# Kernel optimization log

Measured on AMD Instinct MI355X. Metric: run time of the kernel, lower is better.

Reference implementation:

```python
import jax, jax.numpy as jnp
import numpy as np

NB_HEAD = 16
SIZE_PER_HEAD = 64
D_MODEL = 1024
B, S = 4, 2048
NEG_BIG = 1e12  # matches the 1e12 additive-mask constant in the original


def setup_inputs() -> dict:
    key = jax.random.key(0)
    ks = jax.random.split(key, 8)
    Q_seq = jax.random.normal(ks[0], (B, S, D_MODEL), dtype=jnp.float32)
    K_seq = jax.random.normal(ks[1], (B, S, D_MODEL), dtype=jnp.float32)
    V_seq = jax.random.normal(ks[2], (B, S, D_MODEL), dtype=jnp.float32)
    out_dim = NB_HEAD * SIZE_PER_HEAD
    # glorot_uniform-style init
    lim = float(np.sqrt(6.0 / (D_MODEL + out_dim)))
    WQ = jax.random.uniform(ks[3], (D_MODEL, out_dim), minval=-lim, maxval=lim, dtype=jnp.float32)
    WK = jax.random.uniform(ks[4], (D_MODEL, out_dim), minval=-lim, maxval=lim, dtype=jnp.float32)
    WV = jax.random.uniform(ks[5], (D_MODEL, out_dim), minval=-lim, maxval=lim, dtype=jnp.float32)
    Q_len = jax.random.randint(ks[6], (B, 1), 1, S + 1, dtype=jnp.int32)
    V_len = jax.random.randint(ks[7], (B, 1), 1, S + 1, dtype=jnp.int32)
    return {"Q_seq": Q_seq, "K_seq": K_seq, "V_seq": V_seq,
            "WQ": WQ, "WK": WK, "WV": WV, "Q_len": Q_len, "V_len": V_len}


def _len_mask(lengths, seqlen, dtype):
    # one_hot(L) then 1 - cumsum along seq == (pos < L); L >= seqlen -> all ones
    return (jnp.arange(seqlen)[None, :] < lengths[:, 0][:, None]).astype(dtype)


def reference(Q_seq, K_seq, V_seq, WQ, WK, WV, Q_len, V_len):
    b, s, _ = Q_seq.shape
    h, dh = NB_HEAD, SIZE_PER_HEAD
    q = (Q_seq @ WQ).reshape(b, s, h, dh).transpose(0, 2, 1, 3)  # [B,H,S,Dh]
    k = (K_seq @ WK).reshape(b, s, h, dh).transpose(0, 2, 1, 3)
    v = (V_seq @ WV).reshape(b, s, h, dh).transpose(0, 2, 1, 3)
    scores = jnp.einsum('bhqd,bhkd->bhqk', q, k) / jnp.sqrt(jnp.float32(dh))
    mask_k = _len_mask(V_len, s, scores.dtype)  # [B,Sk]
    scores = scores - (1.0 - mask_k)[:, None, None, :] * NEG_BIG
    A = jax.nn.softmax(scores, axis=-1)
    o = jnp.einsum('bhqk,bhkd->bhqd', A, v)
    o = o.transpose(0, 2, 1, 3).reshape(b, s, h * dh)  # [B,S,D]
    mask_q = _len_mask(Q_len, s, o.dtype)
    return o * mask_q[:, :, None]
```

## Files before the change

kernel.cpp:

```cpp
#include <hip/hip_runtime.h>
#include <stdint.h>

typedef __attribute__((ext_vector_type(4))) float f32x4;
typedef __attribute__((ext_vector_type(8))) short bf16x8;
typedef __attribute__((ext_vector_type(4))) unsigned short u16x4;

#define MFMA16(a, b, c) __builtin_amdgcn_mfma_f32_16x16x32_bf16((a), (b), (c), 0, 0, 0)

static __device__ __forceinline__ unsigned short f2bf(float x) {
  union { float f; unsigned int u; } v; v.f = x;
  unsigned int r = v.u + 0x7fffu + ((v.u >> 16) & 1u);
  return (unsigned short)(r >> 16);
}

static __device__ __forceinline__ void gload_lds16(const void* g, void* l) {
  __builtin_amdgcn_global_load_lds(
      (__attribute__((address_space(1))) void*)(g),
      (__attribute__((address_space(3))) void*)(l), 16, 0, 0);
}

template <int CTRL>
static __device__ __forceinline__ float dpp_mov(float x) {
  union { float f; int i; } u, r;
  u.f = x;
  r.i = __builtin_amdgcn_update_dpp(u.i, u.i, CTRL, 0xF, 0xF, false);
  return r.f;
}
static __device__ __forceinline__ float dpp_max16(float x) {
  x = fmaxf(x, dpp_mov<0xB1>(x));
  x = fmaxf(x, dpp_mov<0x4E>(x));
  x = fmaxf(x, dpp_mov<0x124>(x));
  x = fmaxf(x, dpp_mov<0x128>(x));
  return x;
}
static __device__ __forceinline__ float dpp_sum16(float x) {
  x += dpp_mov<0xB1>(x);
  x += dpp_mov<0x4E>(x);
  x += dpp_mov<0x124>(x);
  x += dpp_mov<0x128>(x);
  return x;
}

__global__ void fill_kernel(float* p, int n, float v) {
  int i = blockIdx.x * blockDim.x + threadIdx.x;
  if (i < n) p[i] = v;
}

__global__ __launch_bounds__(256) void conv3_kernel(
    const float* __restrict__ S0, const float* __restrict__ S1, const float* __restrict__ S2,
    unsigned short* __restrict__ D0, unsigned short* __restrict__ D1,
    unsigned short* __restrict__ D2,
    const int* __restrict__ Qlen, const int* __restrict__ Vlen)
{
  const int y = blockIdx.y;
  {
    const int m0 = blockIdx.x * 4;
    const int b = m0 >> 11, s0 = m0 & 2047;
    const int L = (y == 0) ? Qlen[b] : Vlen[b];
    if (s0 >= ((L + 63) & ~63)) return;
  }
  const float* in = (y == 0) ? S0 : (y == 1) ? S1 : S2;
  unsigned short* outp = (y == 0) ? D0 : (y == 1) ? D1 : D2;
  const size_t base = ((size_t)blockIdx.x * 256 + threadIdx.x) * 16;
  const f32x4 a0 = *(const f32x4*)&in[base];
  const f32x4 a1 = *(const f32x4*)&in[base + 4];
  const f32x4 a2 = *(const f32x4*)&in[base + 8];
  const f32x4 a3 = *(const f32x4*)&in[base + 12];
  bf16x8 p0, p1;
#pragma unroll
  for (int u = 0; u < 4; ++u) {
    p0[u]     = (short)f2bf(a0[u]);
    p0[u + 4] = (short)f2bf(a1[u]);
    p1[u]     = (short)f2bf(a2[u]);
    p1[u + 4] = (short)f2bf(a3[u]);
  }
  *(bf16x8*)&outp[base]     = p0;
  *(bf16x8*)&outp[base + 8] = p1;
}

__global__ __launch_bounds__(256) void conv_kernel(
    const float* __restrict__ in, unsigned short* __restrict__ outp)
{
  const size_t base = ((size_t)blockIdx.x * 256 + threadIdx.x) * 16;
  const f32x4 a0 = *(const f32x4*)&in[base];
  const f32x4 a1 = *(const f32x4*)&in[base + 4];
  const f32x4 a2 = *(const f32x4*)&in[base + 8];
  const f32x4 a3 = *(const f32x4*)&in[base + 12];
  bf16x8 p0, p1;
#pragma unroll
  for (int u = 0; u < 4; ++u) {
    p0[u]     = (short)f2bf(a0[u]);
    p0[u + 4] = (short)f2bf(a1[u]);
    p1[u]     = (short)f2bf(a2[u]);
    p1[u + 4] = (short)f2bf(a3[u]);
  }
  *(bf16x8*)&outp[base]     = p0;
  *(bf16x8*)&outp[base + 8] = p1;
}

__global__ __launch_bounds__(256) void wtrans_kernel(
    const float* __restrict__ W0, const float* __restrict__ W1, const float* __restrict__ W2,
    unsigned short* __restrict__ T0, unsigned short* __restrict__ T1, unsigned short* __restrict__ T2)
{
  __shared__ __align__(16) float tile[64][65];
  const float* W = (blockIdx.z == 0) ? W0 : (blockIdx.z == 1) ? W1 : W2;
  unsigned short* T = (blockIdx.z == 0) ? T0 : (blockIdx.z == 1) ? T1 : T2;
  const int t = threadIdx.x;
  const int kb = blockIdx.x * 64, nb = blockIdx.y * 64;
  const int rr = t >> 4, cc = (t & 15) * 4;
#pragma unroll
  for (int p = 0; p < 4; ++p) {
    const int r = rr + p * 16;
    const f32x4 v = *(const f32x4*)&W[(size_t)(kb + r) * 1024 + nb + cc];
#pragma unroll
    for (int j = 0; j < 4; ++j) tile[r][cc + j] = v[j];
  }
  __syncthreads();
#pragma unroll
  for (int p = 0; p < 4; ++p) {
    const int n = rr + p * 16;
    u16x4 o;
#pragma unroll
    for (int j = 0; j < 4; ++j) o[j] = f2bf(tile[cc + j][n]);
    *(u16x4*)&T[(size_t)(nb + n) * 1024 + kb + cc] = o;
  }
}

__global__ __launch_bounds__(256) void proj_gemm_kernel(
    const unsigned short* __restrict__ A0, const unsigned short* __restrict__ A1,
    const unsigned short* __restrict__ A2,
    const unsigned short* __restrict__ B0, const unsigned short* __restrict__ B1,
    const unsigned short* __restrict__ B2,
    unsigned short* __restrict__ O0, unsigned short* __restrict__ O1,
    unsigned short* __restrict__ O2, int zbase,
    const int* __restrict__ Qlen, const int* __restrict__ Vlen)
{
  const int z = blockIdx.z + zbase;
  const int mm = (blockIdx.x + 8 * blockIdx.y + 24 * z) & 63;
  const int m0 = mm * 128, n0 = blockIdx.y * 128;

  {
    const int b = m0 >> 11, s0 = m0 & 2047;
    const int L = (z == 0) ? Qlen[b] : Vlen[b];
    if (s0 >= ((L + 63) & ~63)) return;
  }

  const unsigned short* Ab = (z == 0) ? A0 : (z == 1) ? A1 : A2;
  const unsigned short* Bt = (z == 0) ? B0 : (z == 1) ? B1 : B2;
  unsigned short* outp = (z == 0) ? O0 : (z == 1) ? O1 : O2;
  const float scale = (z == 0) ? 0.125f : 1.0f;

  __shared__ __align__(16) unsigned short Alds[4][128 * 32];
  __shared__ __align__(16) unsigned short Blds[4][128 * 32];
  const int t = threadIdx.x;
  const int lane = t & 63, w = t >> 6;
  const int wr = w >> 1, wc = w & 1;

  f32x4 acc[4][4] = {};

  const int L0 = t, L1 = t + 256;
  const int r0 = L0 >> 2, c0 = ((L0 & 3) ^ ((r0 >> 1) & 3)) * 8;
  const int r1 = L1 >> 2, c1 = ((L1 & 3) ^ ((r1 >> 1) & 3)) * 8;

#define PROJ_STAGE(tile, buf)                                                        \
  do {                                                                               \
    const int kt_ = (tile) * 32;                                                     \
    gload_lds16(&Ab[(size_t)(m0 + r0) * 1024 + kt_ + c0], &Alds[(buf)][L0 * 8]);     \
    gload_lds16(&Bt[(size_t)(n0 + r0) * 1024 + kt_ + c0], &Blds[(buf)][L0 * 8]);     \
    gload_lds16(&Ab[(size_t)(m0 + r1) * 1024 + kt_ + c1], &Alds[(buf)][L1 * 8]);     \
    gload_lds16(&Bt[(size_t)(n0 + r1) * 1024 + kt_ + c1], &Blds[(buf)][L1 * 8]);     \
  } while (0)

  PROJ_STAGE(0, 0);
  PROJ_STAGE(1, 1);
  PROJ_STAGE(2, 2);
  asm volatile("s_waitcnt vmcnt(8)" ::: "memory");
  __builtin_amdgcn_s_barrier();
  __builtin_amdgcn_sched_barrier(0);

  for (int tt = 0; tt < 32; ++tt) {
    const int cur = tt & 3;
    if (tt + 3 < 32) PROJ_STAGE(tt + 3, (tt + 3) & 3);

    const int q = lane >> 4;
    bf16x8 af[4], bfv[4];
#pragma unroll
    for (int m = 0; m < 4; ++m) {
      const int row = wr * 64 + m * 16 + (lane & 15);
      af[m] = *(const bf16x8*)&Alds[cur][row * 32 + ((q ^ ((row >> 1) & 3)) * 8)];
    }
#pragma unroll
    for (int n = 0; n < 4; ++n) {
      const int row = wc * 64 + n * 16 + (lane & 15);
      bfv[n] = *(const bf16x8*)&Blds[cur][row * 32 + ((q ^ ((row >> 1) & 3)) * 8)];
    }
    __builtin_amdgcn_s_setprio(1);
#pragma unroll
    for (int m = 0; m < 4; ++m)
#pragma unroll
      for (int n = 0; n < 4; ++n)
        acc[m][n] = MFMA16(af[m], bfv[n], acc[m][n]);
    __builtin_amdgcn_s_setprio(0);

    if (tt < 29)       asm volatile("s_waitcnt vmcnt(8)" ::: "memory");
    else if (tt == 29) asm volatile("s_waitcnt vmcnt(4)" ::: "memory");
    else               asm volatile("s_waitcnt vmcnt(0)" ::: "memory");
    __builtin_amdgcn_s_barrier();
    __builtin_amdgcn_sched_barrier(0);
  }
#undef PROJ_STAGE

#pragma unroll
  for (int mi = 0; mi < 4; ++mi) {
#pragma unroll
    for (int ni = 0; ni < 4; ++ni) {
      const int nn = n0 + wc * 64 + ni * 16 + (lane & 15);
      const int h = nn >> 6, d = nn & 63;
      const int mbase = m0 + wr * 64 + mi * 16 + ((lane >> 4) << 2);
      const int b = mbase >> 11;
      const int s = mbase & 2047;
      if (z != 2) {
#pragma unroll
        for (int j = 0; j < 4; ++j)
          outp[((size_t)(b * 16 + h) * 2048 + (s + j)) * 64 + d] = f2bf(acc[mi][ni][j] * scale);
      } else {
        u16x4 o;
#pragma unroll
        for (int j = 0; j < 4; ++j) o[j] = f2bf(acc[mi][ni][j]);
        *(u16x4*)&outp[((size_t)(b * 16 + h) * 64 + d) * 2048 + s] = o;
      }
    }
  }
}

__global__ __launch_bounds__(256) void attn_kernel(
    const unsigned short* __restrict__ qa, const unsigned short* __restrict__ ka,
    const unsigned short* __restrict__ va, const int* __restrict__ Qlen,
    const int* __restrict__ Vlen, float* __restrict__ outp)
{
  __shared__ __align__(16) unsigned short Klds[2][64 * 64];
  __shared__ __align__(16) unsigned short Vlds[2][64 * 64];
  __shared__ __align__(16) unsigned short Plds[4][16 * 64];
  const int t = threadIdx.x, lane = t & 63, w = t >> 6;
  const int bh = blockIdx.y, b = bh >> 4, h = bh & 15;
  const int q0 = blockIdx.x * 64;
  const int Lq = Qlen[b], Lv = Vlen[b];
  float* outb = outp + (size_t)b * 2048 * 1024 + h * 64;

  if (q0 >= Lq) {
    const int r = t >> 2, c0 = (t & 3) * 16;
    const f32x4 z = {0.f, 0.f, 0.f, 0.f};
#pragma unroll
    for (int j = 0; j < 4; ++j)
      *(f32x4*)&outb[(size_t)(q0 + r) * 1024 + c0 + j * 4] = z;
    return;
  }

  const unsigned short* qb = qa + (size_t)bh * 2048 * 64;
  const unsigned short* kb = ka + (size_t)bh * 2048 * 64;
  const unsigned short* vb = va + (size_t)bh * 64 * 2048;

  const int sr0 = t >> 3, sc0 = t & 7;
  const int sr1 = (t + 256) >> 3, sc1 = (t + 256) & 7;
  const int sd0 = sr0 * 64 + ((sc0 ^ (sr0 & 7)) * 8);
  const int sd1 = sr1 * 64 + ((sc1 ^ (sr1 & 7)) * 8);

  bf16x8 aq[2];
  {
    const int qrow = q0 + w * 16 + (lane & 15);
#pragma unroll
    for (int f = 0; f < 2; ++f)
      aq[f] = *(const bf16x8*)&qb[(size_t)qrow * 64 + (lane >> 4) * 8 + f * 32];
  }

  float m_run[4], l_run[4];
  f32x4 acc_o[4] = {};
#pragma unroll
  for (int j = 0; j < 4; ++j) { m_run[j] = -3.0e38f; l_run[j] = 0.0f; }

  const int nt = (Lv + 63) >> 6;

  bf16x8 kr0 = *(const bf16x8*)&kb[(size_t)sr0 * 64 + sc0 * 8];
  bf16x8 kr1 = *(const bf16x8*)&kb[(size_t)sr1 * 64 + sc1 * 8];
  bf16x8 vr0 = *(const bf16x8*)&vb[(size_t)sr0 * 2048 + sc0 * 8];
  bf16x8 vr1 = *(const bf16x8*)&vb[(size_t)sr1 * 2048 + sc1 * 8];
  *(bf16x8*)&Klds[0][sd0] = kr0;  *(bf16x8*)&Klds[0][sd1] = kr1;
  *(bf16x8*)&Vlds[0][sd0] = vr0;  *(bf16x8*)&Vlds[0][sd1] = vr1;

  for (int kt = 0; kt < nt; ++kt) {
    __syncthreads();
    const int cur = kt & 1;
    const unsigned short* Kc = &Klds[cur][0];
    const unsigned short* Vc = &Vlds[cur][0];
    const int k0 = kt * 64;

    const bool more = (kt + 1) < nt;
    if (more) {
      const int kn = k0 + 64;
      kr0 = *(const bf16x8*)&kb[(size_t)(kn + sr0) * 64 + sc0 * 8];
      kr1 = *(const bf16x8*)&kb[(size_t)(kn + sr1) * 64 + sc1 * 8];
      vr0 = *(const bf16x8*)&vb[(size_t)sr0 * 2048 + kn + sc0 * 8];
      vr1 = *(const bf16x8*)&vb[(size_t)sr1 * 2048 + kn + sc1 * 8];
    }

    f32x4 s4[4];
    __builtin_amdgcn_s_setprio(1);
#pragma unroll
    for (int kbk = 0; kbk < 4; ++kbk) {
      const int row = kbk * 16 + (lane & 15);
      f32x4 acc = {0.f, 0.f, 0.f, 0.f};
#pragma unroll
      for (int ds = 0; ds < 2; ++ds) {
        const int col = (((lane >> 4) * 8) + ds * 32) ^ ((row & 7) << 3);
        const bf16x8 bk = *(const bf16x8*)&Kc[row * 64 + col];
        acc = MFMA16(aq[ds], bk, acc);
      }
      if (k0 + row >= Lv) {
#pragma unroll
        for (int j = 0; j < 4; ++j) acc[j] = -1e30f;
      }
      s4[kbk] = acc;
    }
    __builtin_amdgcn_s_setprio(0);

    float mn[4], esc[4];
#pragma unroll
    for (int j = 0; j < 4; ++j) {
      float rm = fmaxf(fmaxf(s4[0][j], s4[1][j]), fmaxf(s4[2][j], s4[3][j]));
      rm = dpp_max16(rm);
      mn[j] = fmaxf(m_run[j], rm);
      esc[j] = __expf(m_run[j] - mn[j]);
      m_run[j] = mn[j];
    }

    float p[4][4];
    float rs[4] = {0.f, 0.f, 0.f, 0.f};
#pragma unroll
    for (int kbk = 0; kbk < 4; ++kbk)
#pragma unroll
      for (int j = 0; j < 4; ++j) {
        p[kbk][j] = __expf(s4[kbk][j] - mn[j]);
        rs[j] += p[kbk][j];
      }

    unsigned short* pl = &Plds[w][0];
#pragma unroll
    for (int kbk = 0; kbk < 4; ++kbk)
#pragma unroll
      for (int j = 0; j < 4; ++j) {
        const int row = (lane >> 4) * 4 + j;
        const int col = (kbk * 16 + (lane & 15)) ^ ((row & 7) << 3);
        pl[row * 64 + col] = f2bf(p[kbk][j]);
      }

#pragma unroll
    for (int j = 0; j < 4; ++j) {
      const float s = dpp_sum16(rs[j]);
      l_run[j] = l_run[j] * esc[j] + s;
    }
#pragma unroll
    for (int d = 0; d < 4; ++d)
#pragma unroll
      for (int j = 0; j < 4; ++j) acc_o[d][j] *= esc[j];

    bf16x8 pf[2];
#pragma unroll
    for (int ks = 0; ks < 2; ++ks) {
      const int row = lane & 15;
      const int col = ((lane >> 4) * 8 + ks * 32) ^ ((row & 7) << 3);
      pf[ks] = *(const bf16x8*)&pl[row * 64 + col];
    }

    __builtin_amdgcn_s_setprio(1);
#pragma unroll
    for (int db = 0; db < 4; ++db) {
#pragma unroll
      for (int ks = 0; ks < 2; ++ks) {
        const int vrow = db * 16 + (lane & 15);
        const int vcol = ((lane >> 4) * 8 + ks * 32) ^ ((vrow & 7) << 3);
        const bf16x8 vf = *(const bf16x8*)&Vc[vrow * 64 + vcol];
        acc_o[db] = MFMA16(pf[ks], vf, acc_o[db]);
      }
    }
    __builtin_amdgcn_s_setprio(0);

    if (more) {
      unsigned short* Kn = &Klds[cur ^ 1][0];
      unsigned short* Vn = &Vlds[cur ^ 1][0];
      *(bf16x8*)&Kn[sd0] = kr0;  *(bf16x8*)&Kn[sd1] = kr1;
      *(bf16x8*)&Vn[sd0] = vr0;  *(bf16x8*)&Vn[sd1] = vr1;
    }
  }

#pragma unroll
  for (int j = 0; j < 4; ++j) {
    const int row = q0 + w * 16 + (lane >> 4) * 4 + j;
    const float rl = 1.0f / l_run[j];
#pragma unroll
    for (int db = 0; db < 4; ++db) {
      const float v = acc_o[db][j] * rl;
      outb[(size_t)row * 1024 + db * 16 + (lane & 15)] = (row < Lq) ? v : 0.0f;
    }
  }
}

extern "C" void kernel_launch(void* const* d_in, const int* in_sizes, int n_in,
                              void* d_out, int out_size, void* d_ws, size_t ws_size,
                              hipStream_t stream) {
  float* out = (float*)d_out;

  const float* Qs = (const float*)d_in[0];
  const float* Ks = (const float*)d_in[1];
  const float* Vs = (const float*)d_in[2];
  const float* WQ = (const float*)d_in[3];
  const float* WK = (const float*)d_in[4];
  const float* WV = (const float*)d_in[5];
  const int* Qlen = (const int*)d_in[6];
  const int* Vlen = (const int*)d_in[7];

  unsigned short* WQt = (unsigned short*)d_ws;
  unsigned short* WKt = WQt + (size_t)1024 * 1024;
  unsigned short* WVt = WKt + (size_t)1024 * 1024;
  unsigned short* qa  = WVt + (size_t)1024 * 1024;
  unsigned short* ka  = qa + (size_t)8192 * 1024;
  unsigned short* va  = ka + (size_t)8192 * 1024;
  unsigned short* ext = va + (size_t)8192 * 1024;

  unsigned short* cA = (unsigned short*)d_out;
  unsigned short* cB = cA + (size_t)8192 * 1024;

  const size_t base_need = ((size_t)3 * 1024 * 1024 + (size_t)3 * 8192 * 1024) * 2;
  const size_t ext_need  = base_need + (size_t)8192 * 1024 * 2;

  if (ws_size < base_need) {
    fill_kernel<<<(out_size + 255) / 256, 256, 0, stream>>>(out, out_size, 256.0f);
    return;
  }

  wtrans_kernel<<<dim3(16, 16, 3), 256, 0, stream>>>(WQ, WK, WV, WQt, WKt, WVt);

  if (ws_size >= ext_need) {
    conv3_kernel<<<dim3(2048, 3), 256, 0, stream>>>(Qs, Ks, Vs, cA, cB, ext, Qlen, Vlen);
    proj_gemm_kernel<<<dim3(64, 8, 3), 256, 0, stream>>>(
        cA, cB, ext, WQt, WKt, WVt, qa, ka, va, 0, Qlen, Vlen);
  } else {
    conv_kernel<<<2048, 256, 0, stream>>>(Qs, cA);
    conv_kernel<<<2048, 256, 0, stream>>>(Ks, cB);
    proj_gemm_kernel<<<dim3(64, 8, 2), 256, 0, stream>>>(
        cA, cB, cB, WQt, WKt, WVt, qa, ka, va, 0, Qlen, Vlen);
    conv_kernel<<<2048, 256, 0, stream>>>(Vs, cA);
    proj_gemm_kernel<<<dim3(64, 8, 1), 256, 0, stream>>>(
        cA, cA, cA, WQt, WKt, WVt, qa, ka, va, 2, Qlen, Vlen);
  }
  attn_kernel<<<dim3(32, 64), 256, 0, stream>>>(qa, ka, va, Qlen, Vlen, out);
}
```

Before: 128.0 us.

## Process two 64-row query groups per attention block to reuse K/V tiles

Each attention block now handles 128 query rows, as two groups of 64 that share the same K/V LDS tiles. The grid is halved, so each K/V tile loaded from global memory feeds twice as many rows of QK and PV MFMA work. The cost is roughly double the accumulator and state registers per thread, which lowers occupancy and halves the number of blocks. Work also becomes coarser, since a block with one group past Lq still computes it and only zeroes the output rows at the end. The P scratch buffer in LDS is reused between the two groups within a wave.

```diff
diff --git a/kernel.cpp b/kernel.cpp
--- a/kernel.cpp
+++ b/kernel.cpp
@@ -243,7 +243,7 @@
   __shared__ __align__(16) unsigned short Plds[4][16 * 64];
   const int t = threadIdx.x, lane = t & 63, w = t >> 6;
   const int bh = blockIdx.y, b = bh >> 4, h = bh & 15;
-  const int q0 = blockIdx.x * 64;
+  const int q0 = blockIdx.x * 128;
   const int Lq = Qlen[b], Lv = Vlen[b];
   float* outb = outp + (size_t)b * 2048 * 1024 + h * 64;
 
@@ -251,8 +251,10 @@
     const int r = t >> 2, c0 = (t & 3) * 16;
     const f32x4 z = {0.f, 0.f, 0.f, 0.f};
 #pragma unroll
-    for (int j = 0; j < 4; ++j)
-      *(f32x4*)&outb[(size_t)(q0 + r) * 1024 + c0 + j * 4] = z;
+    for (int jj = 0; jj < 2; ++jj)
+#pragma unroll
+      for (int j = 0; j < 4; ++j)
+        *(f32x4*)&outb[(size_t)(q0 + jj * 64 + r) * 1024 + c0 + j * 4] = z;
     return;
   }
 
@@ -265,18 +267,21 @@
   const int sd0 = sr0 * 64 + ((sc0 ^ (sr0 & 7)) * 8);
   const int sd1 = sr1 * 64 + ((sc1 ^ (sr1 & 7)) * 8);
 
-  bf16x8 aq[2];
-  {
-    const int qrow = q0 + w * 16 + (lane & 15);
+  bf16x8 aq[2][2];
+#pragma unroll
+  for (int g = 0; g < 2; ++g) {
+    const int qrow = q0 + g * 64 + w * 16 + (lane & 15);
 #pragma unroll
     for (int f = 0; f < 2; ++f)
-      aq[f] = *(const bf16x8*)&qb[(size_t)qrow * 64 + (lane >> 4) * 8 + f * 32];
-  }
-
-  float m_run[4], l_run[4];
-  f32x4 acc_o[4] = {};
-#pragma unroll
-  for (int j = 0; j < 4; ++j) { m_run[j] = -3.0e38f; l_run[j] = 0.0f; }
+      aq[g][f] = *(const bf16x8*)&qb[(size_t)qrow * 64 + (lane >> 4) * 8 + f * 32];
+  }
+
+  float m_run[2][4], l_run[2][4];
+  f32x4 acc_o[2][4] = {};
+#pragma unroll
+  for (int g = 0; g < 2; ++g)
+#pragma unroll
+    for (int j = 0; j < 4; ++j) { m_run[g][j] = -3.0e38f; l_run[g][j] = 0.0f; }
 
   const int nt = (Lv + 63) >> 6;
 
@@ -303,86 +308,89 @@
       vr1 = *(const bf16x8*)&vb[(size_t)sr1 * 2048 + kn + sc1 * 8];
     }
 
-    f32x4 s4[4];
-    __builtin_amdgcn_s_setprio(1);
-#pragma unroll
-    for (int kbk = 0; kbk < 4; ++kbk) {
-      const int row = kbk * 16 + (lane & 15);
-      f32x4 acc = {0.f, 0.f, 0.f, 0.f};
-#pragma unroll
-      for (int ds = 0; ds < 2; ++ds) {
-        const int col = (((lane >> 4) * 8) + ds * 32) ^ ((row & 7) << 3);
-        const bf16x8 bk = *(const bf16x8*)&Kc[row * 64 + col];
-        acc = MFMA16(aq[ds], bk, acc);
-      }
-      if (k0 + row >= Lv) {
-#pragma unroll
-        for (int j = 0; j < 4; ++j) acc[j] = -1e30f;
-      }
-      s4[kbk] = acc;
-    }
-    __builtin_amdgcn_s_setprio(0);
-
-    float mn[4], esc[4];
-#pragma unroll
-    for (int j = 0; j < 4; ++j) {
-      float rm = fmaxf(fmaxf(s4[0][j], s4[1][j]), fmaxf(s4[2][j], s4[3][j]));
-      rm = dpp_max16(rm);
-      mn[j] = fmaxf(m_run[j], rm);
-      esc[j] = __expf(m_run[j] - mn[j]);
-      m_run[j] = mn[j];
-    }
-
-    float p[4][4];
-    float rs[4] = {0.f, 0.f, 0.f, 0.f};
-#pragma unroll
-    for (int kbk = 0; kbk < 4; ++kbk)
+#pragma unroll
+    for (int g = 0; g < 2; ++g) {
+      f32x4 s4[4];
+      __builtin_amdgcn_s_setprio(1);
+#pragma unroll
+      for (int kbk = 0; kbk < 4; ++kbk) {
+        const int row = kbk * 16 + (lane & 15);
+        f32x4 acc = {0.f, 0.f, 0.f, 0.f};
+#pragma unroll
+        for (int ds = 0; ds < 2; ++ds) {
+          const int col = (((lane >> 4) * 8) + ds * 32) ^ ((row & 7) << 3);
+          const bf16x8 bk = *(const bf16x8*)&Kc[row * 64 + col];
+          acc = MFMA16(aq[g][ds], bk, acc);
+        }
+        if (k0 + row >= Lv) {
+#pragma unroll
+          for (int j = 0; j < 4; ++j) acc[j] = -1e30f;
+        }
+        s4[kbk] = acc;
+      }
+      __builtin_amdgcn_s_setprio(0);
+
+      float mn[4], esc[4];
 #pragma unroll
       for (int j = 0; j < 4; ++j) {
-        p[kbk][j] = __expf(s4[kbk][j] - mn[j]);
-        rs[j] += p[kbk][j];
-      }
-
-    unsigned short* pl = &Plds[w][0];
-#pragma unroll
-    for (int kbk = 0; kbk < 4; ++kbk)
+        float rm = fmaxf(fmaxf(s4[0][j], s4[1][j]), fmaxf(s4[2][j], s4[3][j]));
+        rm = dpp_max16(rm);
+        mn[j] = fmaxf(m_run[g][j], rm);
+        esc[j] = __expf(m_run[g][j] - mn[j]);
+        m_run[g][j] = mn[j];
+      }
+
+      float p[4][4];
+      float rs[4] = {0.f, 0.f, 0.f, 0.f};
+#pragma unroll
+      for (int kbk = 0; kbk < 4; ++kbk)
+#pragma unroll
+        for (int j = 0; j < 4; ++j) {
+          p[kbk][j] = __expf(s4[kbk][j] - mn[j]);
+          rs[j] += p[kbk][j];
+        }
+
+      unsigned short* pl = &Plds[w][0];
+#pragma unroll
+      for (int kbk = 0; kbk < 4; ++kbk)
+#pragma unroll
+        for (int j = 0; j < 4; ++j) {
+          const int row = (lane >> 4) * 4 + j;
+          const int col = (kbk * 16 + (lane & 15)) ^ ((row & 7) << 3);
+          pl[row * 64 + col] = f2bf(p[kbk][j]);
+        }
+
 #pragma unroll
       for (int j = 0; j < 4; ++j) {
-        const int row = (lane >> 4) * 4 + j;
-        const int col = (kbk * 16 + (lane & 15)) ^ ((row & 7) << 3);
-        pl[row * 64 + col] = f2bf(p[kbk][j]);
-      }
-
-#pragma unroll
-    for (int j = 0; j < 4; ++j) {
-      const float s = dpp_sum16(rs[j]);
-      l_run[j] = l_run[j] * esc[j] + s;
-    }
-#pragma unroll
-    for (int d = 0; d < 4; ++d)
-#pragma unroll
-      for (int j = 0; j < 4; ++j) acc_o[d][j] *= esc[j];
-
-    bf16x8 pf[2];
-#pragma unroll
-    for (int ks = 0; ks < 2; ++ks) {
-      const int row = lane & 15;
-      const int col = ((lane >> 4) * 8 + ks * 32) ^ ((row & 7) << 3);
-      pf[ks] = *(const bf16x8*)&pl[row * 64 + col];
-    }
-
-    __builtin_amdgcn_s_setprio(1);
-#pragma unroll
-    for (int db = 0; db < 4; ++db) {
+        const float s = dpp_sum16(rs[j]);
+        l_run[g][j] = l_run[g][j] * esc[j] + s;
+      }
+#pragma unroll
+      for (int d = 0; d < 4; ++d)
+#pragma unroll
+        for (int j = 0; j < 4; ++j) acc_o[g][d][j] *= esc[j];
+
+      bf16x8 pf[2];
 #pragma unroll
       for (int ks = 0; ks < 2; ++ks) {
-        const int vrow = db * 16 + (lane & 15);
-        const int vcol = ((lane >> 4) * 8 + ks * 32) ^ ((vrow & 7) << 3);
-        const bf16x8 vf = *(const bf16x8*)&Vc[vrow * 64 + vcol];
-        acc_o[db] = MFMA16(pf[ks], vf, acc_o[db]);
-      }
-    }
-    __builtin_amdgcn_s_setprio(0);
+        const int row = lane & 15;
+        const int col = ((lane >> 4) * 8 + ks * 32) ^ ((row & 7) << 3);
+        pf[ks] = *(const bf16x8*)&pl[row * 64 + col];
+      }
+
+      __builtin_amdgcn_s_setprio(1);
+#pragma unroll
+      for (int db = 0; db < 4; ++db) {
+#pragma unroll
+        for (int ks = 0; ks < 2; ++ks) {
+          const int vrow = db * 16 + (lane & 15);
+          const int vcol = ((lane >> 4) * 8 + ks * 32) ^ ((vrow & 7) << 3);
+          const bf16x8 vf = *(const bf16x8*)&Vc[vrow * 64 + vcol];
+          acc_o[g][db] = MFMA16(pf[ks], vf, acc_o[g][db]);
+        }
+      }
+      __builtin_amdgcn_s_setprio(0);
+    }
 
     if (more) {
       unsigned short* Kn = &Klds[cur ^ 1][0];
@@ -393,15 +401,17 @@
   }
 
 #pragma unroll
-  for (int j = 0; j < 4; ++j) {
-    const int row = q0 + w * 16 + (lane >> 4) * 4 + j;
-    const float rl = 1.0f / l_run[j];
-#pragma unroll
-    for (int db = 0; db < 4; ++db) {
-      const float v = acc_o[db][j] * rl;
-      outb[(size_t)row * 1024 + db * 16 + (lane & 15)] = (row < Lq) ? v : 0.0f;
-    }
-  }
+  for (int g = 0; g < 2; ++g)
+#pragma unroll
+    for (int j = 0; j < 4; ++j) {
+      const int row = q0 + g * 64 + w * 16 + (lane >> 4) * 4 + j;
+      const float rl = 1.0f / l_run[g][j];
+#pragma unroll
+      for (int db = 0; db < 4; ++db) {
+        const float v = acc_o[g][db][j] * rl;
+        outb[(size_t)row * 1024 + db * 16 + (lane & 15)] = (row < Lq) ? v : 0.0f;
+      }
+    }
 }
 
 extern "C" void kernel_launch(void* const* d_in, const int* in_sizes, int n_in,
@@ -452,5 +462,5 @@
     proj_gemm_kernel<<<dim3(64, 8, 1), 256, 0, stream>>>(
         cA, cA, cA, WQt, WKt, WVt, qa, ka, va, 2, Qlen, Vlen);
   }
-  attn_kernel<<<dim3(32, 64), 256, 0, stream>>>(qa, ka, va, Qlen, Vlen, out);
-}
+  attn_kernel<<<dim3(16, 64), 256, 0, stream>>>(qa, ka, va, Qlen, Vlen, out);
+}
```

New measurement: 131.8 us. 1.03x slower.

## Split KV across waves in attention with per-wave LDS and final merge

Applied to the files above, without the earlier changes.

Each attention block now processes 16 query rows instead of 64, with its four waves each handling an interleaved subset of 32-key tiles using private LDS buffers, then merging partial softmax states (max, sum, accumulator) through shared memory. This removes the per-iteration block barrier and increases grid parallelism. In exchange, K/V tiles are reloaded for every 16 query rows, quadrupling K/V traffic, and a final cross-wave reduction is added.

```diff
diff --git a/kernel.cpp b/kernel.cpp
--- a/kernel.cpp
+++ b/kernel.cpp
@@ -238,21 +238,17 @@
     const unsigned short* __restrict__ va, const int* __restrict__ Qlen,
     const int* __restrict__ Vlen, float* __restrict__ outp)
 {
-  __shared__ __align__(16) unsigned short Klds[2][64 * 64];
-  __shared__ __align__(16) unsigned short Vlds[2][64 * 64];
-  __shared__ __align__(16) unsigned short Plds[4][16 * 64];
+  __shared__ __align__(16) unsigned char smem[36864];
   const int t = threadIdx.x, lane = t & 63, w = t >> 6;
   const int bh = blockIdx.y, b = bh >> 4, h = bh & 15;
-  const int q0 = blockIdx.x * 64;
+  const int q0 = blockIdx.x * 16;
   const int Lq = Qlen[b], Lv = Vlen[b];
   float* outb = outp + (size_t)b * 2048 * 1024 + h * 64;
 
   if (q0 >= Lq) {
-    const int r = t >> 2, c0 = (t & 3) * 16;
+    const int r = t >> 4, c0 = (t & 15) * 4;
     const f32x4 z = {0.f, 0.f, 0.f, 0.f};
-#pragma unroll
-    for (int j = 0; j < 4; ++j)
-      *(f32x4*)&outb[(size_t)(q0 + r) * 1024 + c0 + j * 4] = z;
+    *(f32x4*)&outb[(size_t)(q0 + r) * 1024 + c0] = z;
     return;
   }
 
@@ -260,14 +256,13 @@
   const unsigned short* kb = ka + (size_t)bh * 2048 * 64;
   const unsigned short* vb = va + (size_t)bh * 64 * 2048;
 
-  const int sr0 = t >> 3, sc0 = t & 7;
-  const int sr1 = (t + 256) >> 3, sc1 = (t + 256) & 7;
-  const int sd0 = sr0 * 64 + ((sc0 ^ (sr0 & 7)) * 8);
-  const int sd1 = sr1 * 64 + ((sc1 ^ (sr1 & 7)) * 8);
+  unsigned short* Klds = (unsigned short*)(smem + w * 9216);
+  unsigned short* Vlds = (unsigned short*)(smem + w * 9216 + 4096);
+  unsigned short* Plds = (unsigned short*)(smem + w * 9216 + 8192);
 
   bf16x8 aq[2];
   {
-    const int qrow = q0 + w * 16 + (lane & 15);
+    const int qrow = q0 + (lane & 15);
 #pragma unroll
     for (int f = 0; f < 2; ++f)
       aq[f] = *(const bf16x8*)&qb[(size_t)qrow * 64 + (lane >> 4) * 8 + f * 32];
@@ -278,41 +273,51 @@
 #pragma unroll
   for (int j = 0; j < 4; ++j) { m_run[j] = -3.0e38f; l_run[j] = 0.0f; }
 
-  const int nt = (Lv + 63) >> 6;
-
-  bf16x8 kr0 = *(const bf16x8*)&kb[(size_t)sr0 * 64 + sc0 * 8];
-  bf16x8 kr1 = *(const bf16x8*)&kb[(size_t)sr1 * 64 + sc1 * 8];
-  bf16x8 vr0 = *(const bf16x8*)&vb[(size_t)sr0 * 2048 + sc0 * 8];
-  bf16x8 vr1 = *(const bf16x8*)&vb[(size_t)sr1 * 2048 + sc1 * 8];
-  *(bf16x8*)&Klds[0][sd0] = kr0;  *(bf16x8*)&Klds[0][sd1] = kr1;
-  *(bf16x8*)&Vlds[0][sd0] = vr0;  *(bf16x8*)&Vlds[0][sd1] = vr1;
-
-  for (int kt = 0; kt < nt; ++kt) {
-    __syncthreads();
-    const int cur = kt & 1;
-    const unsigned short* Kc = &Klds[cur][0];
-    const unsigned short* Vc = &Vlds[cur][0];
-    const int k0 = kt * 64;
-
-    const bool more = (kt + 1) < nt;
+  const int nt = (Lv + 31) >> 5;
+
+  bf16x8 krg[4], vrg[4];
+  int kt = w;
+  if (kt < nt) {
+    const int k0 = kt * 32;
+#pragma unroll
+    for (int i = 0; i < 4; ++i) {
+      const int ci = lane + i * 64;
+      krg[i] = *(const bf16x8*)&kb[(size_t)(k0 + (ci >> 3)) * 64 + (ci & 7) * 8];
+      vrg[i] = *(const bf16x8*)&vb[(size_t)(ci >> 2) * 2048 + k0 + (ci & 3) * 8];
+    }
+#pragma unroll
+    for (int i = 0; i < 4; ++i) {
+      const int ci = lane + i * 64;
+      const int kr = ci >> 3, kc = ci & 7;
+      const int vr = ci >> 2, vc = ci & 3;
+      *(bf16x8*)&Klds[kr * 64 + ((kc ^ (kr & 7)) * 8)] = krg[i];
+      *(bf16x8*)&Vlds[vr * 32 + ((vc ^ (vr & 3)) * 8)] = vrg[i];
+    }
+  }
+
+  for (; kt < nt; kt += 4) {
+    const int k0 = kt * 32;
+    const bool more = (kt + 4) < nt;
     if (more) {
-      const int kn = k0 + 64;
-      kr0 = *(const bf16x8*)&kb[(size_t)(kn + sr0) * 64 + sc0 * 8];
-      kr1 = *(const bf16x8*)&kb[(size_t)(kn + sr1) * 64 + sc1 * 8];
-      vr0 = *(const bf16x8*)&vb[(size_t)sr0 * 2048 + kn + sc0 * 8];
-      vr1 = *(const bf16x8*)&vb[(size_t)sr1 * 2048 + kn + sc1 * 8];
-    }
-
-    f32x4 s4[4];
+      const int kn = k0 + 128;
+#pragma unroll
+      for (int i = 0; i < 4; ++i) {
+        const int ci = lane + i * 64;
+        krg[i] = *(const bf16x8*)&kb[(size_t)(kn + (ci >> 3)) * 64 + (ci & 7) * 8];
+        vrg[i] = *(const bf16x8*)&vb[(size_t)(ci >> 2) * 2048 + kn + (ci & 3) * 8];
+      }
+    }
+
+    f32x4 s4[2];
     __builtin_amdgcn_s_setprio(1);
 #pragma unroll
-    for (int kbk = 0; kbk < 4; ++kbk) {
+    for (int kbk = 0; kbk < 2; ++kbk) {
       const int row = kbk * 16 + (lane & 15);
       f32x4 acc = {0.f, 0.f, 0.f, 0.f};
 #pragma unroll
       for (int ds = 0; ds < 2; ++ds) {
         const int col = (((lane >> 4) * 8) + ds * 32) ^ ((row & 7) << 3);
-        const bf16x8 bk = *(const bf16x8*)&Kc[row * 64 + col];
+        const bf16x8 bk = *(const bf16x8*)&Klds[row * 64 + col];
         acc = MFMA16(aq[ds], bk, acc);
       }
       if (k0 + row >= Lv) {
@@ -326,31 +331,30 @@
     float mn[4], esc[4];
 #pragma unroll
     for (int j = 0; j < 4; ++j) {
-      float rm = fmaxf(fmaxf(s4[0][j], s4[1][j]), fmaxf(s4[2][j], s4[3][j]));
+      float rm = fmaxf(s4[0][j], s4[1][j]);
       rm = dpp_max16(rm);
       mn[j] = fmaxf(m_run[j], rm);
       esc[j] = __expf(m_run[j] - mn[j]);
       m_run[j] = mn[j];
     }
 
-    float p[4][4];
+    float p[2][4];
     float rs[4] = {0.f, 0.f, 0.f, 0.f};
 #pragma unroll
-    for (int kbk = 0; kbk < 4; ++kbk)
+    for (int kbk = 0; kbk < 2; ++kbk)
 #pragma unroll
       for (int j = 0; j < 4; ++j) {
         p[kbk][j] = __expf(s4[kbk][j] - mn[j]);
         rs[j] += p[kbk][j];
       }
 
-    unsigned short* pl = &Plds[w][0];
-#pragma unroll
-    for (int kbk = 0; kbk < 4; ++kbk)
+#pragma unroll
+    for (int kbk = 0; kbk < 2; ++kbk)
 #pragma unroll
       for (int j = 0; j < 4; ++j) {
         const int row = (lane >> 4) * 4 + j;
-        const int col = (kbk * 16 + (lane & 15)) ^ ((row & 7) << 3);
-        pl[row * 64 + col] = f2bf(p[kbk][j]);
+        const int pcol = kbk * 16 + (lane & 15);
+        Plds[row * 32 + (((pcol >> 3) ^ (row & 3)) * 8) + (pcol & 7)] = f2bf(p[kbk][j]);
       }
 
 #pragma unroll
@@ -363,43 +367,72 @@
 #pragma unroll
       for (int j = 0; j < 4; ++j) acc_o[d][j] *= esc[j];
 
-    bf16x8 pf[2];
-#pragma unroll
-    for (int ks = 0; ks < 2; ++ks) {
+    bf16x8 pf;
+    {
       const int row = lane & 15;
-      const int col = ((lane >> 4) * 8 + ks * 32) ^ ((row & 7) << 3);
-      pf[ks] = *(const bf16x8*)&pl[row * 64 + col];
+      pf = *(const bf16x8*)&Plds[row * 32 + (((lane >> 4) ^ (row & 3)) * 8)];
     }
 
     __builtin_amdgcn_s_setprio(1);
 #pragma unroll
     for (int db = 0; db < 4; ++db) {
-#pragma unroll
-      for (int ks = 0; ks < 2; ++ks) {
-        const int vrow = db * 16 + (lane & 15);
-        const int vcol = ((lane >> 4) * 8 + ks * 32) ^ ((vrow & 7) << 3);
-        const bf16x8 vf = *(const bf16x8*)&Vc[vrow * 64 + vcol];
-        acc_o[db] = MFMA16(pf[ks], vf, acc_o[db]);
-      }
+      const int vrow = db * 16 + (lane & 15);
+      const int vch = (lane >> 4) ^ (vrow & 3);
+      const bf16x8 vf = *(const bf16x8*)&Vlds[vrow * 32 + vch * 8];
+      acc_o[db] = MFMA16(pf, vf, acc_o[db]);
     }
     __builtin_amdgcn_s_setprio(0);
 
     if (more) {
-      unsigned short* Kn = &Klds[cur ^ 1][0];
-      unsigned short* Vn = &Vlds[cur ^ 1][0];
-      *(bf16x8*)&Kn[sd0] = kr0;  *(bf16x8*)&Kn[sd1] = kr1;
-      *(bf16x8*)&Vn[sd0] = vr0;  *(bf16x8*)&Vn[sd1] = vr1;
-    }
-  }
-
-#pragma unroll
-  for (int j = 0; j < 4; ++j) {
-    const int row = q0 + w * 16 + (lane >> 4) * 4 + j;
-    const float rl = 1.0f / l_run[j];
-#pragma unroll
-    for (int db = 0; db < 4; ++db) {
-      const float v = acc_o[db][j] * rl;
-      outb[(size_t)row * 1024 + db * 16 + (lane & 15)] = (row < Lq) ? v : 0.0f;
+#pragma unroll
+      for (int i = 0; i < 4; ++i) {
+        const int ci = lane + i * 64;
+        const int kr = ci >> 3, kc = ci & 7;
+        const int vr = ci >> 2, vc = ci & 3;
+        *(bf16x8*)&Klds[kr * 64 + ((kc ^ (kr & 7)) * 8)] = krg[i];
+        *(bf16x8*)&Vlds[vr * 32 + ((vc ^ (vr & 3)) * 8)] = vrg[i];
+      }
+    }
+  }
+
+  __syncthreads();
+  float* comb = (float*)smem;
+  {
+    float* my = comb + ((size_t)w * 64 + lane) * 24;
+#pragma unroll
+    for (int j = 0; j < 4; ++j) { my[j] = m_run[j]; my[4 + j] = l_run[j]; }
+#pragma unroll
+    for (int db = 0; db < 4; ++db)
+#pragma unroll
+      for (int j = 0; j < 4; ++j) my[8 + db * 4 + j] = acc_o[db][j];
+  }
+  __syncthreads();
+  if (w == 0) {
+#pragma unroll
+    for (int ww = 1; ww < 4; ++ww) {
+      const float* o = comb + ((size_t)ww * 64 + lane) * 24;
+#pragma unroll
+      for (int j = 0; j < 4; ++j) {
+        const float mo = o[j];
+        const float M = fmaxf(m_run[j], mo);
+        const float e0 = __expf(m_run[j] - M);
+        const float e1 = __expf(mo - M);
+        l_run[j] = l_run[j] * e0 + o[4 + j] * e1;
+#pragma unroll
+        for (int db = 0; db < 4; ++db)
+          acc_o[db][j] = acc_o[db][j] * e0 + o[8 + db * 4 + j] * e1;
+        m_run[j] = M;
+      }
+    }
+#pragma unroll
+    for (int j = 0; j < 4; ++j) {
+      const int row = q0 + (lane >> 4) * 4 + j;
+      const float rl = 1.0f / l_run[j];
+#pragma unroll
+      for (int db = 0; db < 4; ++db) {
+        const float v = acc_o[db][j] * rl;
+        outb[(size_t)row * 1024 + db * 16 + (lane & 15)] = (row < Lq) ? v : 0.0f;
+      }
     }
   }
 }
@@ -452,5 +485,5 @@
     proj_gemm_kernel<<<dim3(64, 8, 1), 256, 0, stream>>>(
         cA, cA, cA, WQt, WKt, WVt, qa, ka, va, 2, Qlen, Vlen);
   }
-  attn_kernel<<<dim3(32, 64), 256, 0, stream>>>(qa, ka, va, Qlen, Vlen, out);
-}
+  attn_kernel<<<dim3(128, 64), 256, 0, stream>>>(qa, ka, va, Qlen, Vlen, out);
+}
```

Measured after the change: 120.3 us. -6.0%, faster.
